# Kernel optimization log

Hardware: AMD Instinct MI355X
Metric: run time of the kernel (lower is better)

Reference implementation:

```python
import jax, jax.numpy as jnp
import numpy as np

HIDDEN = 64
NHEADS = 8
HEAD_DIM = HIDDEN // NHEADS
N_EDGES = 800000
N_NODES = 50000


def setup_inputs() -> dict:
    key = jax.random.key(0)
    k1, k2, k3, k4 = jax.random.split(key, 4)
    keys = jax.random.normal(k1, (N_EDGES, HIDDEN), dtype=jnp.float32)
    queries = jax.random.normal(k2, (N_EDGES, HIDDEN), dtype=jnp.float32)
    values = jax.random.normal(k3, (N_EDGES, HIDDEN), dtype=jnp.float32)
    dst = jax.random.randint(k4, (N_EDGES,), 0, N_NODES, dtype=jnp.int32)
    return {"keys": keys, "queries": queries, "values": values,
            "dst": dst, "num_nodes": N_NODES}


def reference(keys, queries, values, dst, num_nodes):
    E = keys.shape[0]
    temp = HIDDEN ** (-0.5)
    # reshape to (E, H, D) multi-head layout
    k = keys.reshape(E, NHEADS, HEAD_DIM)
    q = queries.reshape(E, NHEADS, HEAD_DIM)
    v = values.reshape(E, NHEADS, HEAD_DIM)
    # edge-wise dot-product score per head, scaled, then LeakyReLU(0.2)
    scores = jnp.sum(k * q, axis=-1) * temp            # (E, H)
    scores = jnp.where(scores >= 0, scores, 0.2 * scores)
    # segment softmax over edges grouped by destination node (dgl.ops.edge_softmax)
    smax = jax.ops.segment_max(scores, dst, num_segments=num_nodes)  # (N, H)
    smax = jnp.where(jnp.isfinite(smax), smax, 0.0)    # nodes with no in-edges
    ex = jnp.exp(scores - smax[dst])                   # (E, H)
    denom = jax.ops.segment_sum(ex, dst, num_segments=num_nodes)    # (N, H)
    weights = ex / denom[dst]                          # (E, H)
    # dropout p=0.0 -> identity; mask/bias are None -> skipped
    weighted = weights[..., None] * v                  # (E, H, D)
    # scatter-sum to destination nodes (dgl.ops.copy_e_sum)
    out = jax.ops.segment_sum(weighted, dst, num_segments=num_nodes)  # (N, H, D)
    return out.reshape(num_nodes, HIDDEN)
```

## Files before the change

### kernel.cpp

```cpp
#include <hip/hip_runtime.h>

#define HIDDEN 64
#define NHEADS 8


__global__ void hist_kernel(const int* __restrict__ dst, int* __restrict__ counts, int E) {
    int i = blockIdx.x * blockDim.x + threadIdx.x;
    if (i < E) atomicAdd(&counts[dst[i]], 1);
}

__global__ void scan1_kernel(const int* __restrict__ counts, int* __restrict__ offsets,
                             int* __restrict__ partials, int N) {
    int tid = threadIdx.x, lane = tid & 63, wid = tid >> 6;
    int i = blockIdx.x * 256 + tid;
    int x0 = (i < N) ? counts[i] : 0;
    int x = x0;
    #pragma unroll
    for (int off = 1; off < 64; off <<= 1) {
        int y = __shfl_up(x, off);
        if (lane >= off) x += y;
    }
    __shared__ int wsum[4];
    if (lane == 63) wsum[wid] = x;
    __syncthreads();
    if (tid == 0) {
        int s = 0;
        #pragma unroll
        for (int w2 = 0; w2 < 4; ++w2) { int t = wsum[w2]; wsum[w2] = s; s += t; }
        partials[blockIdx.x] = s;
    }
    __syncthreads();
    if (i < N) offsets[i] = wsum[wid] + (x - x0);
}

__global__ void scan2_kernel(int* __restrict__ partials, int PB) {
    int tid = threadIdx.x, lane = tid & 63, wid = tid >> 6;
    int x0 = (tid < PB) ? partials[tid] : 0;
    int x = x0;
    #pragma unroll
    for (int off = 1; off < 64; off <<= 1) {
        int y = __shfl_up(x, off);
        if (lane >= off) x += y;
    }
    __shared__ int wsum[4];
    if (lane == 63) wsum[wid] = x;
    __syncthreads();
    if (tid == 0) {
        int s = 0;
        #pragma unroll
        for (int w2 = 0; w2 < 4; ++w2) { int t = wsum[w2]; wsum[w2] = s; s += t; }
    }
    __syncthreads();
    if (tid < PB) partials[tid] = wsum[wid] + (x - x0);
}

__global__ void scan3_kernel(int* __restrict__ offsets, int* __restrict__ cursor,
                             const int* __restrict__ partials, int N, int E) {
    int i = blockIdx.x * 256 + threadIdx.x;
    if (i < N) {
        int o = offsets[i] + partials[blockIdx.x];
        offsets[i] = o;
        cursor[i] = o;
    }
    if (i == 0) offsets[N] = E;
}

__global__ void scatter_score_kernel(const float* __restrict__ k,
                                     const float* __restrict__ q,
                                     const int* __restrict__ dst,
                                     int* __restrict__ cursor,
                                     int* __restrict__ edge_ids,
                                     float* __restrict__ ex8, int E) {
    int tid = blockIdx.x * blockDim.x + threadIdx.x;
    int e = tid >> 3, h = tid & 7;
    if (e >= E) return;
    int lane = threadIdx.x & 63;

    const float4* kp = (const float4*)(k + (size_t)e * HIDDEN + h * 8);
    const float4* qp = (const float4*)(q + (size_t)e * HIDDEN + h * 8);
    float4 k0 = kp[0], k1 = kp[1];
    float4 q0 = qp[0], q1 = qp[1];
    float pr = k0.x * q0.x + k0.y * q0.y + k0.z * q0.z + k0.w * q0.w +
               k1.x * q1.x + k1.y * q1.y + k1.z * q1.z + k1.w * q1.w;
    float sc = pr * 0.125f;
    sc = (sc >= 0.f) ? sc : 0.2f * sc;
    float exv = __expf(sc);

    int pos = 0;
    if (h == 0) pos = atomicAdd(&cursor[dst[e]], 1);
    pos = __shfl(pos, lane & ~7);
    if (h == 0) edge_ids[pos] = e;
    ex8[(size_t)pos * 8 + h] = exv;
}

__global__ void gat_gather_kernel(const float* __restrict__ v,
                                  const float* __restrict__ ex8,
                                  const int* __restrict__ offsets,
                                  const int* __restrict__ edge_ids,
                                  float* __restrict__ out, int N) {
    int wgid = blockIdx.x * (blockDim.x >> 6) + (threadIdx.x >> 6);
    if (wgid >= N) return;
    int lane = threadIdx.x & 63;
    int h = lane >> 3;
    int start = offsets[wgid], end = offsets[wgid + 1];
    if (end <= start) {
        out[(size_t)wgid * HIDDEN + lane] = 0.f;
        return;
    }
    float acc = 0.f, den = 0.f;

    for (int cbase = start; cbase < end; cbase += 16) {
        int idx[16];
        int eid[16];
        float w[16], vv[16];
        #pragma unroll
        for (int jj = 0; jj < 16; ++jj) {
            int i0 = cbase + jj;
            idx[jj] = (i0 < end) ? i0 : (end - 1);
        }
        #pragma unroll
        for (int jj = 0; jj < 16; ++jj) eid[jj] = edge_ids[idx[jj]];
        #pragma unroll
        for (int jj = 0; jj < 16; ++jj) {
            w[jj]  = ex8[(size_t)idx[jj] * 8 + h];
            vv[jj] = v[(size_t)eid[jj] * HIDDEN + lane];
        }
        #pragma unroll
        for (int jj = 0; jj < 16; ++jj) {
            float m = (cbase + jj < end) ? w[jj] : 0.f;
            acc = fmaf(m, vv[jj], acc);
            den += m;
        }
    }
    out[(size_t)wgid * HIDDEN + lane] = acc / den;
}

extern "C" void kernel_launch(void* const* d_in, const int* in_sizes, int n_in,
                              void* d_out, int out_size, void* d_ws, size_t ws_size,
                              hipStream_t stream) {
    const float* keys    = (const float*)d_in[0];
    const float* queries = (const float*)d_in[1];
    const float* values  = (const float*)d_in[2];
    const int*   dst     = (const int*)d_in[3];
    int E = in_sizes[0] / HIDDEN;
    int N = out_size / HIDDEN;

    int* counts   = (int*)d_ws;
    int* offsets  = counts + N;
    int* cursor   = offsets + N + 1;
    int* partials = cursor + N;
    int* edge_ids = partials + 256;
    float* ex8    = (float*)(edge_ids + E);
    float* out    = (float*)d_out;

    hipMemsetAsync(counts, 0, (size_t)N * sizeof(int), stream);

    int threads = 256;
    int eb = (E + threads - 1) / threads;
    int nb256 = (N + 255) / 256;
    hist_kernel<<<eb, threads, 0, stream>>>(dst, counts, E);
    scan1_kernel<<<nb256, 256, 0, stream>>>(counts, offsets, partials, N);
    scan2_kernel<<<1, 256, 0, stream>>>(partials, nb256);
    scan3_kernel<<<nb256, 256, 0, stream>>>(offsets, cursor, partials, N, E);

    int ehb = ((E * NHEADS) + threads - 1) / threads;
    scatter_score_kernel<<<ehb, threads, 0, stream>>>(keys, queries, dst,
                                                      cursor, edge_ids, ex8, E);

    int wavesPerBlock = threads / 64;
    int gb = (N + wavesPerBlock - 1) / wavesPerBlock;
    gat_gather_kernel<<<gb, threads, 0, stream>>>(values, ex8, offsets,
                                                  edge_ids, out, N);
}
```

Measured before the change: 207.5 us.

## Split edge scoring from atomic scatter into separate score and permute kernels

Edge score computation moves into a grid-stride kernel with 4-way unrolled independent loads, which writes exp scores in edge order. A separate per-edge kernel then does the atomic cursor increment and copies the 8 scores with float4 stores into the sorted position. The aim is to take the atomic and shuffle dependency off the bandwidth-heavy k/q streaming path. In exchange it adds an extra 25.6 MB write and read of ex_edge and one more kernel launch.

```diff
diff --git a/kernel.cpp b/kernel.cpp
--- a/kernel.cpp
+++ b/kernel.cpp
@@ -65,32 +65,49 @@
     if (i == 0) offsets[N] = E;
 }
 
-__global__ void scatter_score_kernel(const float* __restrict__ k,
-                                     const float* __restrict__ q,
-                                     const int* __restrict__ dst,
-                                     int* __restrict__ cursor,
-                                     int* __restrict__ edge_ids,
-                                     float* __restrict__ ex8, int E) {
-    int tid = blockIdx.x * blockDim.x + threadIdx.x;
-    int e = tid >> 3, h = tid & 7;
+__global__ void score_kernel(const float* __restrict__ k,
+                             const float* __restrict__ q,
+                             float* __restrict__ ex_edge, int E) {
+    int total = E * NHEADS;
+    int nth = gridDim.x * blockDim.x;
+    int tid0 = blockIdx.x * blockDim.x + threadIdx.x;
+
+    for (int base = tid0; base < total; base += nth * 4) {
+        int   idx[4];
+        float pr[4];
+        #pragma unroll
+        for (int j = 0; j < 4; ++j) {
+            int i0 = base + j * nth;
+            idx[j] = (i0 < total) ? i0 : (total - 1);
+            const float4* kp = (const float4*)(k + ((size_t)idx[j] << 3));
+            const float4* qp = (const float4*)(q + ((size_t)idx[j] << 3));
+            float4 k0 = kp[0], k1 = kp[1];
+            float4 q0 = qp[0], q1 = qp[1];
+            pr[j] = k0.x * q0.x + k0.y * q0.y + k0.z * q0.z + k0.w * q0.w +
+                    k1.x * q1.x + k1.y * q1.y + k1.z * q1.z + k1.w * q1.w;
+        }
+        #pragma unroll
+        for (int j = 0; j < 4; ++j) {
+            float sc = pr[j] * 0.125f;
+            sc = (sc >= 0.f) ? sc : 0.2f * sc;
+            ex_edge[idx[j]] = __expf(sc);
+        }
+    }
+}
+
+__global__ void scatter_permute_kernel(const int* __restrict__ dst,
+                                       int* __restrict__ cursor,
+                                       const float* __restrict__ ex_edge,
+                                       int* __restrict__ edge_ids,
+                                       float* __restrict__ ex8, int E) {
+    int e = blockIdx.x * blockDim.x + threadIdx.x;
     if (e >= E) return;
-    int lane = threadIdx.x & 63;
-
-    const float4* kp = (const float4*)(k + (size_t)e * HIDDEN + h * 8);
-    const float4* qp = (const float4*)(q + (size_t)e * HIDDEN + h * 8);
-    float4 k0 = kp[0], k1 = kp[1];
-    float4 q0 = qp[0], q1 = qp[1];
-    float pr = k0.x * q0.x + k0.y * q0.y + k0.z * q0.z + k0.w * q0.w +
-               k1.x * q1.x + k1.y * q1.y + k1.z * q1.z + k1.w * q1.w;
-    float sc = pr * 0.125f;
-    sc = (sc >= 0.f) ? sc : 0.2f * sc;
-    float exv = __expf(sc);
-
-    int pos = 0;
-    if (h == 0) pos = atomicAdd(&cursor[dst[e]], 1);
-    pos = __shfl(pos, lane & ~7);
-    if (h == 0) edge_ids[pos] = e;
-    ex8[(size_t)pos * 8 + h] = exv;
+    float4 a = ((const float4*)ex_edge)[(size_t)e * 2];
+    float4 b = ((const float4*)ex_edge)[(size_t)e * 2 + 1];
+    int pos = atomicAdd(&cursor[dst[e]], 1);
+    edge_ids[pos] = e;
+    ((float4*)ex8)[(size_t)pos * 2]     = a;
+    ((float4*)ex8)[(size_t)pos * 2 + 1] = b;
 }
 
 __global__ void gat_gather_kernel(const float* __restrict__ v,
@@ -145,27 +162,35 @@
     int E = in_sizes[0] / HIDDEN;
     int N = out_size / HIDDEN;
 
-    int* counts   = (int*)d_ws;
+    char* w = (char*)d_ws;
+    int* counts   = (int*)w;
     int* offsets  = counts + N;
     int* cursor   = offsets + N + 1;
     int* partials = cursor + N;
-    int* edge_ids = partials + 256;
-    float* ex8    = (float*)(edge_ids + E);
-    float* out    = (float*)d_out;
+    size_t used = (size_t)(3 * N + 1 + 256) * sizeof(int);
+    used = (used + 15) & ~(size_t)15;
+    int* edge_ids = (int*)(w + used);
+    used += (size_t)E * sizeof(int);
+    used = (used + 15) & ~(size_t)15;
+    float* ex_edge = (float*)(w + used);
+    used += (size_t)E * NHEADS * sizeof(float);
+    float* ex8 = (float*)(w + used);
+    float* out = (float*)d_out;
 
     hipMemsetAsync(counts, 0, (size_t)N * sizeof(int), stream);
 
     int threads = 256;
     int eb = (E + threads - 1) / threads;
     int nb256 = (N + 255) / 256;
+
     hist_kernel<<<eb, threads, 0, stream>>>(dst, counts, E);
     scan1_kernel<<<nb256, 256, 0, stream>>>(counts, offsets, partials, N);
     scan2_kernel<<<1, 256, 0, stream>>>(partials, nb256);
     scan3_kernel<<<nb256, 256, 0, stream>>>(offsets, cursor, partials, N, E);
 
-    int ehb = ((E * NHEADS) + threads - 1) / threads;
-    scatter_score_kernel<<<ehb, threads, 0, stream>>>(keys, queries, dst,
-                                                      cursor, edge_ids, ex8, E);
+    score_kernel<<<1024, threads, 0, stream>>>(keys, queries, ex_edge, E);
+    scatter_permute_kernel<<<eb, threads, 0, stream>>>(dst, cursor, ex_edge,
+                                                       edge_ids, ex8, E);
 
     int wavesPerBlock = threads / 64;
     int gb = (N + wavesPerBlock - 1) / wavesPerBlock;
```

After: 245.2 us. +18.2%, slower.
